# Performance work log

Hardware: AMD Instinct MI355X
Metric: run time of the kernel (lower is better)

## Reference

```python
import jax, jax.numpy as jnp
import numpy as np

B, NR, NP, E, F, EIN, H, OUT = 2, 16384, 65536, 262144, 128, 4, 16, 4
EPS = 1e-6

def _mlp(x, W1, b1, W2, b2):
    return jax.nn.swish(x @ W1 + b1) @ W2 + b2

def _cond_norm(x, tau, C1, c1, C2, c2):
    # conditioned LayerNorm: scale/shift computed from tau by a shallow MLP
    h = jax.nn.swish(tau @ C1 + c1)               # [B, H]
    scale, shift = jnp.split(h @ C2 + c2, 2, -1)  # [B, F] each
    mu = jnp.mean(x, -1, keepdims=True)
    var = jnp.var(x, -1, keepdims=True)
    xn = (x - mu) * jax.lax.rsqrt(var + EPS)
    return xn * (1.0 + scale[:, None, :]) + shift[:, None, :]

def _segment_mean(feat, recv, num_segments):
    seg = lambda f, r: jax.ops.segment_sum(f, r, num_segments=num_segments)
    s = jax.vmap(seg)(feat, recv)
    cnt = jax.vmap(seg)(jnp.ones(recv.shape, feat.dtype), recv)
    return s / jnp.maximum(cnt, 1.0)[..., None]

def setup_inputs():
    key = jax.random.key(0)
    ks = iter(jax.random.split(key, 48))
    dense = lambda i, o: jax.random.normal(next(ks), (i, o), jnp.float32) / np.sqrt(i)
    inp = {}
    inp['rnode_features'] = jax.random.normal(next(ks), (B, NR, F), jnp.float32)
    inp['pnode_features'] = jax.random.normal(next(ks), (B, NP, F), jnp.float32)
    inp['edge_features'] = jax.random.normal(next(ks), (B, E, EIN), jnp.float32)
    inp['tau'] = jax.random.uniform(next(ks), (B, 1), jnp.float32)
    # edge embedding MLP + cond norm
    inp['We1'], inp['We2'] = dense(EIN, F), dense(F, F)
    inp['be1'], inp['be2'] = jnp.zeros((F,)), jnp.zeros((F,))
    inp['Ce1'], inp['Ce2'] = dense(1, H), dense(H, 2 * F)
    inp['ce1'], inp['ce2'] = jnp.zeros((H,)), jnp.zeros((2 * F,))
    # edge update MLP + cond norm
    inp['Wu1'], inp['Wu2'] = dense(3 * F, F), dense(F, F)
    inp['bu1'], inp['bu2'] = jnp.zeros((F,)), jnp.zeros((F,))
    inp['Cu1'], inp['Cu2'] = dense(1, H), dense(H, 2 * F)
    inp['cu1'], inp['cu2'] = jnp.zeros((H,)), jnp.zeros((2 * F,))
    # pnode update MLP + cond norm
    inp['Wp1'], inp['Wp2'] = dense(2 * F, F), dense(F, F)
    inp['bp1'], inp['bp2'] = jnp.zeros((F,)), jnp.zeros((F,))
    inp['Cp1'], inp['Cp2'] = dense(1, H), dense(H, 2 * F)
    inp['cp1'], inp['cp2'] = jnp.zeros((H,)), jnp.zeros((2 * F,))
    # rnode update MLP + cond norm
    inp['Wr1'], inp['Wr2'] = dense(F, F), dense(F, F)
    inp['br1'], inp['br2'] = jnp.zeros((F,)), jnp.zeros((F,))
    inp['Cr1'], inp['Cr2'] = dense(1, H), dense(H, 2 * F)
    inp['cr1'], inp['cr2'] = jnp.zeros((H,)), jnp.zeros((2 * F,))
    # pnode output MLP (no norm)
    inp['Wo1'], inp['Wo2'] = dense(F, F), dense(F, OUT)
    inp['bo1'], inp['bo2'] = jnp.zeros((F,)), jnp.zeros((OUT,))
    inp['senders'] = jax.random.randint(next(ks), (B, E), 0, NR, jnp.int32)
    inp['receivers'] = jax.random.randint(next(ks), (B, E), 0, NP, jnp.int32)
    return inp

def reference(rnode_features, pnode_features, edge_features, tau,
              We1, be1, We2, be2, Ce1, ce1, Ce2, ce2,
              Wu1, bu1, Wu2, bu2, Cu1, cu1, Cu2, cu2,
              Wp1, bp1, Wp2, bp2, Cp1, cp1, Cp2, cp2,
              Wr1, br1, Wr2, br2, Cr1, cr1, Cr2, cr2,
              Wo1, bo1, Wo2, bo2, senders, receivers):
    # 1) embed raw r2p edge features to latent size (embed_edges=True)
    e = _cond_norm(_mlp(edge_features, We1, be1, We2, be2), tau, Ce1, ce1, Ce2, ce2)
    # 2) one message-passing step: edge update from gathered sender/receiver feats
    sf = jnp.take_along_axis(rnode_features, senders[..., None], axis=1)    # [B,E,F]
    rf = jnp.take_along_axis(pnode_features, receivers[..., None], axis=1)  # [B,E,F]
    e = e + _cond_norm(_mlp(jnp.concatenate([e, sf, rf], -1), Wu1, bu1, Wu2, bu2),
                       tau, Cu1, cu1, Cu2, cu2)
    # 3) pnode update with segment_mean aggregation, residual
    agg = _segment_mean(e, receivers, NP)                                   # [B,NP,F]
    p = pnode_features + _cond_norm(
        _mlp(jnp.concatenate([pnode_features, agg], -1), Wp1, bp1, Wp2, bp2),
        tau, Cp1, cp1, Cp2, cp2)
    # 4) rnode update (no incoming edges; structurally present but unused by output)
    r = rnode_features + _cond_norm(_mlp(rnode_features, Wr1, br1, Wr2, br2),
                                    tau, Cr1, cr1, Cr2, cr2)
    del r
    # 5) output MLP on pnodes (node_output_size=dict(pnodes=num_outputs))
    return _mlp(p, Wo1, bo1, Wo2, bo2)
```

## Files before the change

kernel.cpp:

```cpp
#include <hip/hip_runtime.h>

constexpr int cB  = 2;
constexpr int cNR = 16384;
constexpr int cNP = 65536;
constexpr int cE  = 262144;
constexpr int cF  = 128;
constexpr int cEB = cE / 64;
constexpr int SP  = 136;
constexpr int EFP = 40;

typedef unsigned short u16;
using f32x4 = __attribute__((ext_vector_type(4))) float;
using s8v   = __attribute__((ext_vector_type(8))) short;

constexpr int G8_We2 = 0, G8_Wu1 = 16, G8_Wu2 = 64, G8_Wp1 = 80, G8_Wp2 = 112, G8_Wo1 = 128;
constexpr int G8_TOT = 144;
constexpr int SWZ_N = G8_TOT * 128 + 256 + 512;
constexpr int WB_WE1 = (G8_TOT * 128 + 256) * 8;

constexpr size_t WS_CNT  = 0;
constexpr size_t WS_POS  = WS_CNT + (size_t)cB * cNP;
constexpr size_t WS_BSUM = WS_POS + (size_t)cB * cNP;
constexpr size_t WS_SS   = WS_BSUM + 512;
constexpr size_t WS_WB   = WS_SS + 3 * cB * 256;
constexpr size_t WS_RB   = WS_WB + (size_t)SWZ_N * 4;
constexpr size_t WS_PB   = WS_RB + (size_t)cB * cNR * cF / 2;
constexpr size_t WS_EL   = WS_PB + (size_t)cB * cNP * cF / 2;
constexpr size_t WS_EB   = WS_EL + (size_t)cB * cE;

__device__ __forceinline__ float bf2f(u16 u) {
  union { unsigned int i; float f; } v; v.i = ((unsigned int)u) << 16; return v.f;
}
__device__ __forceinline__ u16 f2bf(float f) {
  union { float f; unsigned int i; } v; v.f = f;
  unsigned int x = v.i;
  return (u16)((x + 0x7fffu + ((x >> 16) & 1u)) >> 16);
}
__device__ __forceinline__ u16 f2bf_fast(float f) {
  return (u16)((__float_as_uint(f) + 0x8000u) >> 16);
}
__device__ __forceinline__ unsigned pack2(float a, float b) {
  return __builtin_amdgcn_perm(__float_as_uint(b) + 0x8000u,
                               __float_as_uint(a) + 0x8000u, 0x07060302u);
}
__device__ __forceinline__ float swishf(float x) {
  return x * __builtin_amdgcn_rcpf(1.0f + __expf(-x));
}

template <int CTRL>
__device__ __forceinline__ float dpp_add(float x) {
  int xi = __float_as_int(x);
  int r = __builtin_amdgcn_update_dpp(xi, xi, CTRL, 0xf, 0xf, false);
  return x + __int_as_float(r);
}

__device__ __forceinline__ void gload4_lds(const u16* gsrc, u16* lds) {
  __builtin_amdgcn_global_load_lds(
      (const __attribute__((address_space(1))) void*)gsrc,
      (__attribute__((address_space(3))) void*)lds, 4, 0, 0);
}

__device__ __forceinline__ void kloop128s(const u16* act, const u16* __restrict__ wbg,
                                          f32x4 (&acc)[4][2], int cw, int l16, int quad) {
  s8v bf[4][2];
#pragma unroll
  for (int k0 = 0; k0 < 4; ++k0)
#pragma unroll
    for (int ci = 0; ci < 2; ++ci)
      bf[k0][ci] = *(const s8v*)(wbg + ((size_t)(k0 * 4 + quad) * 128 + cw + ci * 16 + l16) * 8);
#pragma unroll
  for (int k0 = 0; k0 < 4; ++k0) {
    s8v af[4];
#pragma unroll
    for (int ri = 0; ri < 4; ++ri)
      af[ri] = *(const s8v*)(act + (ri * 16 + l16) * SP + k0 * 32 + quad * 8);
#pragma unroll
    for (int ri = 0; ri < 4; ++ri)
#pragma unroll
      for (int ci = 0; ci < 2; ++ci)
        acc[ri][ci] = __builtin_amdgcn_mfma_f32_16x16x32_bf16(af[ri], bf[k0][ci], acc[ri][ci], 0, 0, 0);
  }
}

__device__ __forceinline__ void init_acc_s(f32x4 (&acc)[4][2], const float* __restrict__ bias,
                                           int cw, int l16) {
#pragma unroll
  for (int ci = 0; ci < 2; ++ci) {
    float bv = bias[cw + ci * 16 + l16];
#pragma unroll
    for (int ri = 0; ri < 4; ++ri) acc[ri][ci] = (f32x4){bv, bv, bv, bv};
  }
}

__device__ __forceinline__ void cond_norm_s(f32x4 (&acc)[4][2], float* red, float* musig,
                                            const float* __restrict__ ssp,
                                            int cw, int l16, int quad, int wv, int t) {
  __syncthreads();
#pragma unroll
  for (int ri = 0; ri < 4; ++ri)
#pragma unroll
    for (int reg = 0; reg < 4; ++reg) {
      float v0 = acc[ri][0][reg], v1 = acc[ri][1][reg];
      float s = v0 + v1;
      float q = v0 * v0 + v1 * v1;
      s = dpp_add<0x128>(s); q = dpp_add<0x128>(q);
      s = dpp_add<0x124>(s); q = dpp_add<0x124>(q);
      s = dpp_add<0x122>(s); q = dpp_add<0x122>(q);
      s = dpp_add<0x121>(s); q = dpp_add<0x121>(q);
      if (l16 == 0) {
        int row = ri * 16 + quad * 4 + reg;
        red[row * 8 + wv * 2]     = s;
        red[row * 8 + wv * 2 + 1] = q;
      }
    }
  __syncthreads();
  if (t < 64) {
    float sum = red[t * 8 + 0] + red[t * 8 + 2] + red[t * 8 + 4] + red[t * 8 + 6];
    float sq  = red[t * 8 + 1] + red[t * 8 + 3] + red[t * 8 + 5] + red[t * 8 + 7];
    float mu  = sum * (1.0f / 128.0f);
    float var = fmaxf(sq * (1.0f / 128.0f) - mu * mu, 0.0f);
    musig[t * 2]     = mu;
    musig[t * 2 + 1] = __builtin_amdgcn_rsqf(var + 1e-6f);
  }
  __syncthreads();
  float scl[2], shf[2];
#pragma unroll
  for (int ci = 0; ci < 2; ++ci) {
    int col = cw + ci * 16 + l16;
    scl[ci] = 1.0f + ssp[col];
    shf[ci] = ssp[128 + col];
  }
#pragma unroll
  for (int ri = 0; ri < 4; ++ri)
#pragma unroll
    for (int reg = 0; reg < 4; ++reg) {
      int row = ri * 16 + quad * 4 + reg;
      float mu = musig[row * 2], is = musig[row * 2 + 1];
#pragma unroll
      for (int ci = 0; ci < 2; ++ci)
        acc[ri][ci][reg] = (acc[ri][ci][reg] - mu) * is * scl[ci] + shf[ci];
    }
}

template <bool DOSWISH>
__device__ __forceinline__ void store_s(u16* buf, const f32x4 (&acc)[4][2],
                                        int cw, int l16, int quad) {
#pragma unroll
  for (int ri = 0; ri < 4; ++ri)
#pragma unroll
    for (int reg = 0; reg < 4; ++reg) {
      int row = ri * 16 + quad * 4 + reg;
#pragma unroll
      for (int ci = 0; ci < 2; ++ci) {
        float v = acc[ri][ci][reg];
        if (DOSWISH) v = swishf(v);
        buf[row * SP + cw + ci * 16 + l16] = f2bf_fast(v);
      }
    }
}

__global__ void zero_kernel(float4* __restrict__ p, int n4) {
  int i = blockIdx.x * 256 + threadIdx.x;
  if (i < n4) p[i] = make_float4(0.f, 0.f, 0.f, 0.f);
}

__global__ void cvtn2_kernel(const float* __restrict__ sa, u16* __restrict__ da, int n2a,
                             const float* __restrict__ sb, u16* __restrict__ db, int n2b) {
  int i = blockIdx.x * 256 + threadIdx.x;
  if (i < n2a) {
    float2 v = ((const float2*)sa)[i];
    ((unsigned*)da)[i] = pack2(v.x, v.y);
  } else if (i < n2a + n2b) {
    int k = i - n2a;
    float2 v = ((const float2*)sb)[k];
    ((unsigned*)db)[k] = pack2(v.x, v.y);
  }
}

__global__ void hist_kernel(const int* __restrict__ receivers, int* __restrict__ cntI) {
  int i = blockIdx.x * 256 + threadIdx.x;
  if (i >= cB * cE) return;
  int b = i / cE;
  int r = min(max(receivers[i], 0), cNP - 1);
  atomicAdd(&cntI[(size_t)b * cNP + r], 1);
}

__global__ void scanA_kernel(const int* __restrict__ cntI, int* __restrict__ bsum) {
  __shared__ int red[256];
  int g = blockIdx.x, t = threadIdx.x;
  red[t] = cntI[g * 256 + t];
  __syncthreads();
  for (int s = 128; s > 0; s >>= 1) {
    if (t < s) red[t] += red[t + s];
    __syncthreads();
  }
  if (t == 0) bsum[g] = red[0];
}

__global__ void scanB_kernel(int* __restrict__ bsum) {
  __shared__ int s0[512], s1[512];
  int t = threadIdx.x;
  int v0 = bsum[t];
  s0[t] = v0;
  __syncthreads();
  int* src = s0; int* dst = s1;
  for (int s = 1; s < 512; s <<= 1) {
    dst[t] = src[t] + ((t >= s) ? src[t - s] : 0);
    __syncthreads();
    int* tmp = src; src = dst; dst = tmp;
  }
  bsum[t] = src[t] - v0;
}

__global__ void scanC_kernel(const int* __restrict__ cntI, const int* __restrict__ bsum,
                             int* __restrict__ pos) {
  __shared__ int s0[256], s1[256];
  int g = blockIdx.x, t = threadIdx.x;
  int v0 = cntI[g * 256 + t];
  s0[t] = v0;
  __syncthreads();
  int* src = s0; int* dst = s1;
  for (int s = 1; s < 256; s <<= 1) {
    dst[t] = src[t] + ((t >= s) ? src[t - s] : 0);
    __syncthreads();
    int* tmp = src; src = dst; dst = tmp;
  }
  pos[g * 256 + t] = src[t] - v0 + bsum[g];
}

__global__ void fill_kernel(const int* __restrict__ receivers, int* __restrict__ pos,
                            int* __restrict__ elist) {
  int i = blockIdx.x * 256 + threadIdx.x;
  if (i >= cB * cE) return;
  int b = i / cE, e = i - b * cE;
  int r = min(max(receivers[i], 0), cNP - 1);
  int idx = atomicAdd(&pos[(size_t)b * cNP + r], 1);
  elist[idx] = e;
}

struct SwzSrc { const float* p[7]; };

__global__ void swz_kernel(SwzSrc s, const float* __restrict__ Wo2, u16* __restrict__ wb) {
  int t = blockIdx.x * 256 + threadIdx.x;
  if (t >= SWZ_N) return;
  if (t >= G8_TOT * 128 + 256) {
    int idx3 = t - (G8_TOT * 128 + 256);
    int k8 = idx3 >> 7, n = idx3 & 127;
    const float* We1 = s.p[6];
    u16 v[8];
#pragma unroll
    for (int j = 0; j < 8; ++j) {
      int k = k8 * 8 + j;
      v[j] = (k < 4) ? f2bf(We1[(size_t)k * 128 + n]) : (u16)0;
    }
    ((uint4*)wb)[t] = *(uint4*)v;
    return;
  }
  if (t >= G8_TOT * 128) {
    int idx2 = t - G8_TOT * 128;
    int k8 = idx2 >> 4, n = idx2 & 15;
    u16 v[8];
#pragma unroll
    for (int j = 0; j < 8; ++j)
      v[j] = (n < 4) ? f2bf(Wo2[(size_t)(k8 * 8 + j) * 4 + n]) : (u16)0;
    ((uint4*)wb)[G8_TOT * 128 + k8 * 16 + n] = *(uint4*)v;
    return;
  }
  int n = t & 127, g8 = t >> 7;
  int seg, base;
  if (g8 < G8_Wu1)      { seg = 0; base = G8_We2; }
  else if (g8 < G8_Wu2) { seg = 1; base = G8_Wu1; }
  else if (g8 < G8_Wp1) { seg = 2; base = G8_Wu2; }
  else if (g8 < G8_Wp2) { seg = 3; base = G8_Wp1; }
  else if (g8 < G8_Wo1) { seg = 4; base = G8_Wp2; }
  else                  { seg = 5; base = G8_Wo1; }
  const float* W = s.p[seg];
  int k8l = g8 - base;
  u16 v[8];
#pragma unroll
  for (int j = 0; j < 8; ++j) {
    int kd = k8l * 8 + j;
    int ks = kd;
    if (seg == 3 && kd >= 128) {
      int p = kd - 128;
      ks = 128 + ((p >> 5) << 5) + ((p & 1) << 4) + ((p & 31) >> 1);
    }
    v[j] = f2bf(W[(size_t)ks * 128 + n]);
  }
  ((uint4*)wb)[g8 * 128 + n] = *(uint4*)v;
}

__global__ void cond_kernel(const float* __restrict__ tau,
                            const float* __restrict__ Ce1, const float* __restrict__ ce1,
                            const float* __restrict__ Ce2, const float* __restrict__ ce2,
                            const float* __restrict__ Cu1, const float* __restrict__ cu1,
                            const float* __restrict__ Cu2, const float* __restrict__ cu2,
                            const float* __restrict__ Cp1, const float* __restrict__ cp1,
                            const float* __restrict__ Cp2, const float* __restrict__ cp2,
                            float* __restrict__ ss) {
  int set = blockIdx.x, b = blockIdx.y, j = threadIdx.x;
  const float *C1, *c1, *C2, *c2;
  if (set == 0)      { C1 = Ce1; c1 = ce1; C2 = Ce2; c2 = ce2; }
  else if (set == 1) { C1 = Cu1; c1 = cu1; C2 = Cu2; c2 = cu2; }
  else               { C1 = Cp1; c1 = cp1; C2 = Cp2; c2 = cp2; }
  float tf = tau[b];
  float a = c2[j];
  for (int k = 0; k < 16; ++k) {
    float h = swishf(tf * C1[k] + c1[k]);
    a = fmaf(h, C2[k * 256 + j], a);
  }
  ss[(size_t)set * cB * 256 + (size_t)b * 256 + j] = a;
}

struct EWb { const float *be1, *be2, *bu1, *bu2; };

struct __align__(16) EdgeSmem {
  u16 bufE[64 * SP];
  u16 bufX[64 * SP];
  union {
    u16 ef[64 * EFP];
    struct { float red[512]; float musig[128]; } r;
  } u;
  int sidx[64], ridx[64];
};

__global__ __launch_bounds__(256, 4) void edge_mfma(
    const u16* __restrict__ rnb, const u16* __restrict__ pnb,
    const float* __restrict__ efeat, const int* __restrict__ senders,
    const int* __restrict__ receivers, const int* __restrict__ elist,
    EWb w, const u16* __restrict__ wb,
    const float* __restrict__ ss, u16* __restrict__ ebuf) {
  __shared__ EdgeSmem sm;
  const int t = threadIdx.x, wv = t >> 6, lane = t & 63, l16 = lane & 15, quad = lane >> 4;
  const int cw = wv * 32;
  const int raw = blockIdx.x;
  const int swz = (raw & 7) * (cB * cEB / 8) + (raw >> 3);
  const int b   = swz / cEB;

  if (t < 64) {
    int eid = elist[(size_t)swz * 64 + t];
    size_t ge = (size_t)b * cE + eid;
    sm.sidx[t] = min(max(senders[ge], 0), cNR - 1);
    sm.ridx[t] = min(max(receivers[ge], 0), cNP - 1);
    float4 ef = *(const float4*)(efeat + ge * 4);
    uint4 w0 = { pack2(ef.x, ef.y), pack2(ef.z, ef.w), 0u, 0u };
    uint4 zz = { 0u, 0u, 0u, 0u };
    uint4* rowp = (uint4*)(sm.u.ef + (size_t)t * EFP);
    rowp[0] = w0; rowp[1] = zz; rowp[2] = zz; rowp[3] = zz; rowp[4] = zz;
  }
  __syncthreads();

  f32x4 acc[4][2];

  init_acc_s(acc, w.be1, cw, l16);
  {
    const u16* wbe1 = wb + WB_WE1;
    s8v bf0 = *(const s8v*)(wbe1 + ((size_t)quad * 128 + cw + l16) * 8);
    s8v bf1 = *(const s8v*)(wbe1 + ((size_t)quad * 128 + cw + 16 + l16) * 8);
#pragma unroll
    for (int ri = 0; ri < 4; ++ri) {
      s8v af = *(const s8v*)(sm.u.ef + (ri * 16 + l16) * EFP + quad * 8);
      acc[ri][0] = __builtin_amdgcn_mfma_f32_16x16x32_bf16(af, bf0, acc[ri][0], 0, 0, 0);
      acc[ri][1] = __builtin_amdgcn_mfma_f32_16x16x32_bf16(af, bf1, acc[ri][1], 0, 0, 0);
    }
  }
  store_s<true>(sm.bufX, acc, cw, l16, quad);
  __syncthreads();

  init_acc_s(acc, w.be2, cw, l16);
  kloop128s(sm.bufX, wb + (size_t)G8_We2 * 1024, acc, cw, l16, quad);
  cond_norm_s(acc, sm.u.r.red, sm.u.r.musig, ss + (size_t)b * 256, cw, l16, quad, wv, t);
  store_s<false>(sm.bufE, acc, cw, l16, quad);

#pragma unroll
  for (int rr = 0; rr < 16; ++rr) {
    int row = wv * 16 + rr;
    int si = __builtin_amdgcn_readfirstlane(sm.sidx[row]);
    gload4_lds(rnb + ((size_t)b * cNR + si) * cF + lane * 2,
               sm.bufX + row * SP);
  }
  f32x4 accU[4][2];
  init_acc_s(accU, w.bu1, cw, l16);
  __syncthreads();
  kloop128s(sm.bufX, wb + (size_t)(G8_Wu1 + 16) * 1024, accU, cw, l16, quad);
  __syncthreads();
#pragma unroll
  for (int rr = 0; rr < 16; ++rr) {
    int row = wv * 16 + rr;
    int ri_ = __builtin_amdgcn_readfirstlane(sm.ridx[row]);
    gload4_lds(pnb + ((size_t)b * cNP + ri_) * cF + lane * 2,
               sm.bufX + row * SP);
  }
  kloop128s(sm.bufE, wb + (size_t)G8_Wu1 * 1024, accU, cw, l16, quad);
  __syncthreads();
  kloop128s(sm.bufX, wb + (size_t)(G8_Wu1 + 32) * 1024, accU, cw, l16, quad);
  __syncthreads();
  store_s<true>(sm.bufX, accU, cw, l16, quad);
  __syncthreads();

  init_acc_s(acc, w.bu2, cw, l16);
  kloop128s(sm.bufX, wb + (size_t)G8_Wu2 * 1024, acc, cw, l16, quad);
  cond_norm_s(acc, sm.u.r.red, sm.u.r.musig, ss + (size_t)(cB + b) * 256, cw, l16, quad, wv, t);

  {
    unsigned* eb32o = (unsigned*)ebuf + (size_t)(swz * 64) * 64;
#pragma unroll
    for (int ri = 0; ri < 4; ++ri)
#pragma unroll
      for (int reg = 0; reg < 4; ++reg) {
        int row = ri * 16 + quad * 4 + reg;
        float v0 = acc[ri][0][reg] + bf2f(sm.bufE[row * SP + cw + l16]);
        float v1 = acc[ri][1][reg] + bf2f(sm.bufE[row * SP + cw + 16 + l16]);
        eb32o[(size_t)row * 64 + wv * 16 + l16] = pack2(v0, v1);
      }
  }
}

struct PWb { const float *bp1, *bp2, *bo1, *bo2; };

struct __align__(16) PnodeSmem {
  u16 bufP[64 * SP];
  u16 bufX[64 * SP];
  float red[512];
  float musig[128];
  float cinv[64];
  int startA[64];
  int endA[72];
};

__global__ __launch_bounds__(256, 4) void pnode_mfma(
    const u16* __restrict__ pnb, PWb w, const u16* __restrict__ wb,
    const float* __restrict__ ss, const unsigned* __restrict__ eb32,
    const int* __restrict__ cntI, const int* __restrict__ pos,
    float* __restrict__ out) {
  __shared__ PnodeSmem sm;
  const int t = threadIdx.x, wv = t >> 6, lane = t & 63, l16 = lane & 15, quad = lane >> 4;
  const int cw = wv * 32;
  const int b  = blockIdx.y;
  const int n0 = blockIdx.x * 64;

  if (t < 64) {
    size_t g = (size_t)b * cNP + n0 + t;
    int c  = cntI[g];
    int e_ = pos[g];
    sm.startA[t] = e_ - c;
    sm.endA[t]   = e_;
    sm.cinv[t]   = __builtin_amdgcn_rcpf(fmaxf((float)c, 1.0f));
  } else if (t < 72) {
    sm.endA[t] = 0x7fffffff;
  }
  __syncthreads();

#pragma unroll
  for (int rr = 0; rr < 16; ++rr) {
    int row = wv * 16 + rr;
    unsigned pvu = *(const unsigned*)(pnb + (((size_t)b * cNP + n0 + row) * cF + lane * 2));
    *(unsigned*)(sm.bufP + row * SP + lane * 2) = pvu;
  }

  {
    const int nodeLo = wv * 16;
    int cur  = nodeLo;
    int bnd  = __builtin_amdgcn_readfirstlane(sm.endA[cur]);
    int s    = __builtin_amdgcn_readfirstlane(sm.startA[nodeLo]);
    const int sEnd = __builtin_amdgcn_readfirstlane(sm.endA[nodeLo + 15]);
    float a0 = 0.f, a1 = 0.f;
    for (; s < sEnd; s += 8) {
      unsigned v[8];
      int m = sEnd - s;
#pragma unroll
      for (int j = 0; j < 8; ++j)
        if (j < m) v[j] = eb32[(size_t)(s + j) * 64 + lane];
#pragma unroll
      for (int j = 0; j < 8; ++j) {
        if (j < m) {
          while (s + j == bnd) {
            float ci = sm.cinv[cur];
            *(unsigned*)(sm.bufX + cur * SP + lane * 2) = pack2(a0 * ci, a1 * ci);
            a0 = a1 = 0.f; ++cur;
            bnd = __builtin_amdgcn_readfirstlane(sm.endA[cur]);
          }
          a0 += bf2f((u16)(v[j] & 0xffffu));
          a1 += bf2f((u16)(v[j] >> 16));
        }
      }
    }
    while (cur < nodeLo + 16) {
      float ci = sm.cinv[cur];
      *(unsigned*)(sm.bufX + cur * SP + lane * 2) = pack2(a0 * ci, a1 * ci);
      a0 = a1 = 0.f; ++cur;
    }
  }
  __syncthreads();

  f32x4 acc[4][2];

  init_acc_s(acc, w.bp1, cw, l16);
  kloop128s(sm.bufP, wb + (size_t)G8_Wp1 * 1024, acc, cw, l16, quad);
  kloop128s(sm.bufX, wb + (size_t)(G8_Wp1 + 16) * 1024, acc, cw, l16, quad);
  __syncthreads();
  store_s<true>(sm.bufX, acc, cw, l16, quad);
  __syncthreads();

  init_acc_s(acc, w.bp2, cw, l16);
  kloop128s(sm.bufX, wb + (size_t)G8_Wp2 * 1024, acc, cw, l16, quad);
  cond_norm_s(acc, sm.red, sm.musig, ss + (size_t)(2 * cB + b) * 256, cw, l16, quad, wv, t);
#pragma unroll
  for (int ri = 0; ri < 4; ++ri)
#pragma unroll
    for (int reg = 0; reg < 4; ++reg) {
      int row = ri * 16 + quad * 4 + reg;
#pragma unroll
      for (int ci = 0; ci < 2; ++ci)
        acc[ri][ci][reg] += bf2f(sm.bufP[row * SP + cw + ci * 16 + l16]);
    }
  __syncthreads();
  store_s<false>(sm.bufP, acc, cw, l16, quad);
  __syncthreads();

  init_acc_s(acc, w.bo1, cw, l16);
  kloop128s(sm.bufP, wb + (size_t)G8_Wo1 * 1024, acc, cw, l16, quad);
  store_s<true>(sm.bufX, acc, cw, l16, quad);
  __syncthreads();

  {
    const u16* wo2 = wb + (size_t)G8_TOT * 1024;
    float bv = (l16 < 4) ? w.bo2[l16] : 0.0f;
    f32x4 a1 = {bv, bv, bv, bv};
#pragma unroll
    for (int k0 = 0; k0 < 4; ++k0) {
      s8v af = *(const s8v*)(sm.bufX + (wv * 16 + l16) * SP + k0 * 32 + quad * 8);
      s8v bf = *(const s8v*)(wo2 + ((size_t)(k0 * 4 + quad) * 16 + l16) * 8);
      a1 = __builtin_amdgcn_mfma_f32_16x16x32_bf16(af, bf, a1, 0, 0, 0);
    }
    if (l16 < 4) {
      size_t obase = (size_t)b * cNP + n0 + wv * 16 + quad * 4;
#pragma unroll
      for (int reg = 0; reg < 4; ++reg)
        out[(obase + reg) * 4 + l16] = a1[reg];
    }
  }
}

extern "C" void kernel_launch(void* const* d_in, const int* in_sizes, int n_in,
                              void* d_out, int out_size, void* d_ws, size_t ws_size,
                              hipStream_t stream) {
  const float* rnode = (const float*)d_in[0];
  const float* pnode = (const float*)d_in[1];
  const float* efeat = (const float*)d_in[2];
  const float* tau   = (const float*)d_in[3];
  const int* senders   = (const int*)d_in[40];
  const int* receivers = (const int*)d_in[41];
  float* ws = (float*)d_ws;
  int* cntI  = (int*)(ws + WS_CNT);
  int* pos   = (int*)(ws + WS_POS);
  int* bsum  = (int*)(ws + WS_BSUM);
  u16* wb    = (u16*)(ws + WS_WB);
  u16* rnb   = (u16*)(ws + WS_RB);
  u16* pnb   = (u16*)(ws + WS_PB);
  int* elist = (int*)(ws + WS_EL);
  u16* ebuf  = (u16*)(ws + WS_EB);

  SwzSrc sw;
  sw.p[0] = (const float*)d_in[5];
  sw.p[1] = (const float*)d_in[12];
  sw.p[2] = (const float*)d_in[13];
  sw.p[3] = (const float*)d_in[20];
  sw.p[4] = (const float*)d_in[21];
  sw.p[5] = (const float*)d_in[36];
  sw.p[6] = (const float*)d_in[4];
  swz_kernel<<<(SWZ_N + 255) / 256, 256, 0, stream>>>(sw, (const float*)d_in[37], wb);

  const int nrn2 = (int)((size_t)cB * cNR * cF / 2);
  const int npn2 = (int)((size_t)cB * cNP * cF / 2);
  cvtn2_kernel<<<(nrn2 + npn2 + 255) / 256, 256, 0, stream>>>(
      rnode, rnb, nrn2, pnode, pnb, npn2);

  cond_kernel<<<dim3(3, cB), 256, 0, stream>>>(
      tau,
      (const float*)d_in[8],  (const float*)d_in[10],
      (const float*)d_in[9],  (const float*)d_in[11],
      (const float*)d_in[16], (const float*)d_in[18],
      (const float*)d_in[17], (const float*)d_in[19],
      (const float*)d_in[24], (const float*)d_in[26],
      (const float*)d_in[25], (const float*)d_in[27],
      ws + WS_SS);

  const int n4 = (int)((size_t)cB * cNP * 4 / 16);
  zero_kernel<<<(n4 + 255) / 256, 256, 0, stream>>>((float4*)cntI, n4);
  const int nBE = cB * cE;
  hist_kernel<<<(nBE + 255) / 256, 256, 0, stream>>>(receivers, cntI);
  scanA_kernel<<<512, 256, 0, stream>>>(cntI, bsum);
  scanB_kernel<<<1, 512, 0, stream>>>(bsum);
  scanC_kernel<<<512, 256, 0, stream>>>(cntI, bsum, pos);
  fill_kernel<<<(nBE + 255) / 256, 256, 0, stream>>>(receivers, pos, elist);

  EWb ew = { (const float*)d_in[6], (const float*)d_in[7],
             (const float*)d_in[14], (const float*)d_in[15] };
  PWb pw = { (const float*)d_in[22], (const float*)d_in[23], (const float*)d_in[38],
             (const float*)d_in[39] };

  edge_mfma<<<dim3(cB * cEB), 256, 0, stream>>>(
      rnb, pnb, efeat, senders, receivers, elist, ew, wb,
      ws + WS_SS, ebuf);

  pnode_mfma<<<dim3(cNP / 64, cB), 256, 0, stream>>>(
      pnb, pw, wb, ws + WS_SS, (const unsigned*)ebuf, cntI, pos,
      (float*)d_out);
}
```

Baseline: 456.4 us.

## Split edge and pnode MFMA work across eight waves with sixteen columns each

The edge and pnode kernels go from 4 waves of 256 threads, each owning 32 output columns, to 8 waves of 512 threads, each owning 16 columns. The reduction buffer grows to hold 8 partial sums, and gathers and segment sums are split over 8 rows per wave. The edge kernel now stages its residual output through LDS and writes rows with coalesced stores instead of scattered packed stores. The Wp1 row permutation is dropped from weight packing, which only stays consistent if that permutation matched the old 2-column interleaved store. The aim is more waves to hide latency, at the cost of more barriers and duplicated activation-fragment loads per MFMA.

```diff
diff --git a/kernel.cpp b/kernel.cpp
--- a/kernel.cpp
+++ b/kernel.cpp
@@ -60,39 +60,30 @@
       (__attribute__((address_space(3))) void*)lds, 4, 0, 0);
 }
 
-__device__ __forceinline__ void kloop128s(const u16* act, const u16* __restrict__ wbg,
-                                          f32x4 (&acc)[4][2], int cw, int l16, int quad) {
-  s8v bf[4][2];
+__device__ __forceinline__ void kloop16(const u16* act, const u16* __restrict__ wbg,
+                                        f32x4 (&acc)[4], int cw, int l16, int quad) {
+  s8v bf[4];
 #pragma unroll
   for (int k0 = 0; k0 < 4; ++k0)
-#pragma unroll
-    for (int ci = 0; ci < 2; ++ci)
-      bf[k0][ci] = *(const s8v*)(wbg + ((size_t)(k0 * 4 + quad) * 128 + cw + ci * 16 + l16) * 8);
+    bf[k0] = *(const s8v*)(wbg + ((size_t)(k0 * 4 + quad) * 128 + cw + l16) * 8);
 #pragma unroll
   for (int k0 = 0; k0 < 4; ++k0) {
-    s8v af[4];
-#pragma unroll
-    for (int ri = 0; ri < 4; ++ri)
-      af[ri] = *(const s8v*)(act + (ri * 16 + l16) * SP + k0 * 32 + quad * 8);
-#pragma unroll
-    for (int ri = 0; ri < 4; ++ri)
-#pragma unroll
-      for (int ci = 0; ci < 2; ++ci)
-        acc[ri][ci] = __builtin_amdgcn_mfma_f32_16x16x32_bf16(af[ri], bf[k0][ci], acc[ri][ci], 0, 0, 0);
-  }
-}
-
-__device__ __forceinline__ void init_acc_s(f32x4 (&acc)[4][2], const float* __restrict__ bias,
+#pragma unroll
+    for (int ri = 0; ri < 4; ++ri) {
+      s8v af = *(const s8v*)(act + (ri * 16 + l16) * SP + k0 * 32 + quad * 8);
+      acc[ri] = __builtin_amdgcn_mfma_f32_16x16x32_bf16(af, bf[k0], acc[ri], 0, 0, 0);
+    }
+  }
+}
+
+__device__ __forceinline__ void init_acc16(f32x4 (&acc)[4], const float* __restrict__ bias,
                                            int cw, int l16) {
-#pragma unroll
-  for (int ci = 0; ci < 2; ++ci) {
-    float bv = bias[cw + ci * 16 + l16];
-#pragma unroll
-    for (int ri = 0; ri < 4; ++ri) acc[ri][ci] = (f32x4){bv, bv, bv, bv};
-  }
-}
-
-__device__ __forceinline__ void cond_norm_s(f32x4 (&acc)[4][2], float* red, float* musig,
+  float bv = bias[cw + l16];
+#pragma unroll
+  for (int ri = 0; ri < 4; ++ri) acc[ri] = (f32x4){bv, bv, bv, bv};
+}
+
+__device__ __forceinline__ void cond_norm16(f32x4 (&acc)[4], float* red, float* musig,
                                             const float* __restrict__ ssp,
                                             int cw, int l16, int quad, int wv, int t) {
   __syncthreads();
@@ -100,62 +91,56 @@
   for (int ri = 0; ri < 4; ++ri)
 #pragma unroll
     for (int reg = 0; reg < 4; ++reg) {
-      float v0 = acc[ri][0][reg], v1 = acc[ri][1][reg];
-      float s = v0 + v1;
-      float q = v0 * v0 + v1 * v1;
+      float v = acc[ri][reg];
+      float s = v;
+      float q = v * v;
       s = dpp_add<0x128>(s); q = dpp_add<0x128>(q);
       s = dpp_add<0x124>(s); q = dpp_add<0x124>(q);
       s = dpp_add<0x122>(s); q = dpp_add<0x122>(q);
       s = dpp_add<0x121>(s); q = dpp_add<0x121>(q);
       if (l16 == 0) {
         int row = ri * 16 + quad * 4 + reg;
-        red[row * 8 + wv * 2]     = s;
-        red[row * 8 + wv * 2 + 1] = q;
+        red[row * 16 + wv * 2]     = s;
+        red[row * 16 + wv * 2 + 1] = q;
       }
     }
   __syncthreads();
   if (t < 64) {
-    float sum = red[t * 8 + 0] + red[t * 8 + 2] + red[t * 8 + 4] + red[t * 8 + 6];
-    float sq  = red[t * 8 + 1] + red[t * 8 + 3] + red[t * 8 + 5] + red[t * 8 + 7];
+    float sum = 0.f, sq = 0.f;
+#pragma unroll
+    for (int w8 = 0; w8 < 8; ++w8) {
+      sum += red[t * 16 + w8 * 2];
+      sq  += red[t * 16 + w8 * 2 + 1];
+    }
     float mu  = sum * (1.0f / 128.0f);
     float var = fmaxf(sq * (1.0f / 128.0f) - mu * mu, 0.0f);
     musig[t * 2]     = mu;
     musig[t * 2 + 1] = __builtin_amdgcn_rsqf(var + 1e-6f);
   }
   __syncthreads();
-  float scl[2], shf[2];
-#pragma unroll
-  for (int ci = 0; ci < 2; ++ci) {
-    int col = cw + ci * 16 + l16;
-    scl[ci] = 1.0f + ssp[col];
-    shf[ci] = ssp[128 + col];
-  }
+  float scl = 1.0f + ssp[cw + l16];
+  float shf = ssp[128 + cw + l16];
 #pragma unroll
   for (int ri = 0; ri < 4; ++ri)
 #pragma unroll
     for (int reg = 0; reg < 4; ++reg) {
       int row = ri * 16 + quad * 4 + reg;
       float mu = musig[row * 2], is = musig[row * 2 + 1];
-#pragma unroll
-      for (int ci = 0; ci < 2; ++ci)
-        acc[ri][ci][reg] = (acc[ri][ci][reg] - mu) * is * scl[ci] + shf[ci];
+      acc[ri][reg] = (acc[ri][reg] - mu) * is * scl + shf;
     }
 }
 
 template <bool DOSWISH>
-__device__ __forceinline__ void store_s(u16* buf, const f32x4 (&acc)[4][2],
+__device__ __forceinline__ void store16(u16* buf, const f32x4 (&acc)[4],
                                         int cw, int l16, int quad) {
 #pragma unroll
   for (int ri = 0; ri < 4; ++ri)
 #pragma unroll
     for (int reg = 0; reg < 4; ++reg) {
       int row = ri * 16 + quad * 4 + reg;
-#pragma unroll
-      for (int ci = 0; ci < 2; ++ci) {
-        float v = acc[ri][ci][reg];
-        if (DOSWISH) v = swishf(v);
-        buf[row * SP + cw + ci * 16 + l16] = f2bf_fast(v);
-      }
+      float v = acc[ri][reg];
+      if (DOSWISH) v = swishf(v);
+      buf[row * SP + cw + l16] = f2bf_fast(v);
     }
 }
 
@@ -278,15 +263,7 @@
   int k8l = g8 - base;
   u16 v[8];
 #pragma unroll
-  for (int j = 0; j < 8; ++j) {
-    int kd = k8l * 8 + j;
-    int ks = kd;
-    if (seg == 3 && kd >= 128) {
-      int p = kd - 128;
-      ks = 128 + ((p >> 5) << 5) + ((p & 1) << 4) + ((p & 31) >> 1);
-    }
-    v[j] = f2bf(W[(size_t)ks * 128 + n]);
-  }
+  for (int j = 0; j < 8; ++j) v[j] = f2bf(W[(size_t)(k8l * 8 + j) * 128 + n]);
   ((uint4*)wb)[g8 * 128 + n] = *(uint4*)v;
 }
 
@@ -319,12 +296,12 @@
   u16 bufX[64 * SP];
   union {
     u16 ef[64 * EFP];
-    struct { float red[512]; float musig[128]; } r;
+    struct { float red[1024]; float musig[128]; } r;
   } u;
   int sidx[64], ridx[64];
 };
 
-__global__ __launch_bounds__(256, 4) void edge_mfma(
+__global__ __launch_bounds__(512, 8) void edge_mfma(
     const u16* __restrict__ rnb, const u16* __restrict__ pnb,
     const float* __restrict__ efeat, const int* __restrict__ senders,
     const int* __restrict__ receivers, const int* __restrict__ elist,
@@ -332,7 +309,7 @@
     const float* __restrict__ ss, u16* __restrict__ ebuf) {
   __shared__ EdgeSmem sm;
   const int t = threadIdx.x, wv = t >> 6, lane = t & 63, l16 = lane & 15, quad = lane >> 4;
-  const int cw = wv * 32;
+  const int cw = wv * 16;
   const int raw = blockIdx.x;
   const int swz = (raw & 7) * (cB * cEB / 8) + (raw >> 3);
   const int b   = swz / cEB;
@@ -350,69 +327,73 @@
   }
   __syncthreads();
 
-  f32x4 acc[4][2];
-
-  init_acc_s(acc, w.be1, cw, l16);
+  f32x4 acc[4];
+
+  init_acc16(acc, w.be1, cw, l16);
   {
     const u16* wbe1 = wb + WB_WE1;
     s8v bf0 = *(const s8v*)(wbe1 + ((size_t)quad * 128 + cw + l16) * 8);
-    s8v bf1 = *(const s8v*)(wbe1 + ((size_t)quad * 128 + cw + 16 + l16) * 8);
 #pragma unroll
     for (int ri = 0; ri < 4; ++ri) {
       s8v af = *(const s8v*)(sm.u.ef + (ri * 16 + l16) * EFP + quad * 8);
-      acc[ri][0] = __builtin_amdgcn_mfma_f32_16x16x32_bf16(af, bf0, acc[ri][0], 0, 0, 0);
-      acc[ri][1] = __builtin_amdgcn_mfma_f32_16x16x32_bf16(af, bf1, acc[ri][1], 0, 0, 0);
-    }
-  }
-  store_s<true>(sm.bufX, acc, cw, l16, quad);
-  __syncthreads();
-
-  init_acc_s(acc, w.be2, cw, l16);
-  kloop128s(sm.bufX, wb + (size_t)G8_We2 * 1024, acc, cw, l16, quad);
-  cond_norm_s(acc, sm.u.r.red, sm.u.r.musig, ss + (size_t)b * 256, cw, l16, quad, wv, t);
-  store_s<false>(sm.bufE, acc, cw, l16, quad);
-
-#pragma unroll
-  for (int rr = 0; rr < 16; ++rr) {
-    int row = wv * 16 + rr;
+      acc[ri] = __builtin_amdgcn_mfma_f32_16x16x32_bf16(af, bf0, acc[ri], 0, 0, 0);
+    }
+  }
+  store16<true>(sm.bufX, acc, cw, l16, quad);
+  __syncthreads();
+
+  init_acc16(acc, w.be2, cw, l16);
+  kloop16(sm.bufX, wb + (size_t)G8_We2 * 1024, acc, cw, l16, quad);
+  cond_norm16(acc, sm.u.r.red, sm.u.r.musig, ss + (size_t)b * 256, cw, l16, quad, wv, t);
+  store16<false>(sm.bufE, acc, cw, l16, quad);
+
+#pragma unroll
+  for (int rr = 0; rr < 8; ++rr) {
+    int row = wv * 8 + rr;
     int si = __builtin_amdgcn_readfirstlane(sm.sidx[row]);
     gload4_lds(rnb + ((size_t)b * cNR + si) * cF + lane * 2,
                sm.bufX + row * SP);
   }
-  f32x4 accU[4][2];
-  init_acc_s(accU, w.bu1, cw, l16);
-  __syncthreads();
-  kloop128s(sm.bufX, wb + (size_t)(G8_Wu1 + 16) * 1024, accU, cw, l16, quad);
-  __syncthreads();
-#pragma unroll
-  for (int rr = 0; rr < 16; ++rr) {
-    int row = wv * 16 + rr;
+  f32x4 accU[4];
+  init_acc16(accU, w.bu1, cw, l16);
+  __syncthreads();
+  kloop16(sm.bufX, wb + (size_t)(G8_Wu1 + 16) * 1024, accU, cw, l16, quad);
+  __syncthreads();
+#pragma unroll
+  for (int rr = 0; rr < 8; ++rr) {
+    int row = wv * 8 + rr;
     int ri_ = __builtin_amdgcn_readfirstlane(sm.ridx[row]);
     gload4_lds(pnb + ((size_t)b * cNP + ri_) * cF + lane * 2,
                sm.bufX + row * SP);
   }
-  kloop128s(sm.bufE, wb + (size_t)G8_Wu1 * 1024, accU, cw, l16, quad);
-  __syncthreads();
-  kloop128s(sm.bufX, wb + (size_t)(G8_Wu1 + 32) * 1024, accU, cw, l16, quad);
-  __syncthreads();
-  store_s<true>(sm.bufX, accU, cw, l16, quad);
-  __syncthreads();
-
-  init_acc_s(acc, w.bu2, cw, l16);
-  kloop128s(sm.bufX, wb + (size_t)G8_Wu2 * 1024, acc, cw, l16, quad);
-  cond_norm_s(acc, sm.u.r.red, sm.u.r.musig, ss + (size_t)(cB + b) * 256, cw, l16, quad, wv, t);
-
+  kloop16(sm.bufE, wb + (size_t)G8_Wu1 * 1024, accU, cw, l16, quad);
+  __syncthreads();
+  kloop16(sm.bufX, wb + (size_t)(G8_Wu1 + 32) * 1024, accU, cw, l16, quad);
+  __syncthreads();
+  store16<true>(sm.bufX, accU, cw, l16, quad);
+  __syncthreads();
+
+  init_acc16(acc, w.bu2, cw, l16);
+  kloop16(sm.bufX, wb + (size_t)G8_Wu2 * 1024, acc, cw, l16, quad);
+  cond_norm16(acc, sm.u.r.red, sm.u.r.musig, ss + (size_t)(cB + b) * 256, cw, l16, quad, wv, t);
+
+#pragma unroll
+  for (int ri = 0; ri < 4; ++ri)
+#pragma unroll
+    for (int reg = 0; reg < 4; ++reg) {
+      int row = ri * 16 + quad * 4 + reg;
+      acc[ri][reg] += bf2f(sm.bufE[row * SP + cw + l16]);
+    }
+  store16<false>(sm.bufX, acc, cw, l16, quad);
+  __syncthreads();
   {
     unsigned* eb32o = (unsigned*)ebuf + (size_t)(swz * 64) * 64;
 #pragma unroll
-    for (int ri = 0; ri < 4; ++ri)
-#pragma unroll
-      for (int reg = 0; reg < 4; ++reg) {
-        int row = ri * 16 + quad * 4 + reg;
-        float v0 = acc[ri][0][reg] + bf2f(sm.bufE[row * SP + cw + l16]);
-        float v1 = acc[ri][1][reg] + bf2f(sm.bufE[row * SP + cw + 16 + l16]);
-        eb32o[(size_t)row * 64 + wv * 16 + l16] = pack2(v0, v1);
-      }
+    for (int rr = 0; rr < 8; ++rr) {
+      int row = wv * 8 + rr;
+      unsigned v = *(const unsigned*)(sm.bufX + row * SP + lane * 2);
+      eb32o[(size_t)row * 64 + lane] = v;
+    }
   }
 }
 
@@ -421,21 +402,21 @@
 struct __align__(16) PnodeSmem {
   u16 bufP[64 * SP];
   u16 bufX[64 * SP];
-  float red[512];
+  float red[1024];
   float musig[128];
   float cinv[64];
   int startA[64];
   int endA[72];
 };
 
-__global__ __launch_bounds__(256, 4) void pnode_mfma(
+__global__ __launch_bounds__(512, 8) void pnode_mfma(
     const u16* __restrict__ pnb, PWb w, const u16* __restrict__ wb,
     const float* __restrict__ ss, const unsigned* __restrict__ eb32,
     const int* __restrict__ cntI, const int* __restrict__ pos,
     float* __restrict__ out) {
   __shared__ PnodeSmem sm;
   const int t = threadIdx.x, wv = t >> 6, lane = t & 63, l16 = lane & 15, quad = lane >> 4;
-  const int cw = wv * 32;
+  const int cw = wv * 16;
   const int b  = blockIdx.y;
   const int n0 = blockIdx.x * 64;
 
@@ -452,18 +433,18 @@
   __syncthreads();
 
 #pragma unroll
-  for (int rr = 0; rr < 16; ++rr) {
-    int row = wv * 16 + rr;
+  for (int rr = 0; rr < 8; ++rr) {
+    int row = wv * 8 + rr;
     unsigned pvu = *(const unsigned*)(pnb + (((size_t)b * cNP + n0 + row) * cF + lane * 2));
     *(unsigned*)(sm.bufP + row * SP + lane * 2) = pvu;
   }
 
   {
-    const int nodeLo = wv * 16;
+    const int nodeLo = wv * 8;
     int cur  = nodeLo;
     int bnd  = __builtin_amdgcn_readfirstlane(sm.endA[cur]);
     int s    = __builtin_amdgcn_readfirstlane(sm.startA[nodeLo]);
-    const int sEnd = __builtin_amdgcn_readfirstlane(sm.endA[nodeLo + 15]);
+    const int sEnd = __builtin_amdgcn_readfirstlane(sm.endA[nodeLo + 7]);
     float a0 = 0.f, a1 = 0.f;
     for (; s < sEnd; s += 8) {
       unsigned v[8];
@@ -485,7 +466,7 @@
         }
       }
     }
-    while (cur < nodeLo + 16) {
+    while (cur < nodeLo + 8) {
       float ci = sm.cinv[cur];
       *(unsigned*)(sm.bufX + cur * SP + lane * 2) = pack2(a0 * ci, a1 * ci);
       a0 = a1 = 0.f; ++cur;
@@ -493,37 +474,35 @@
   }
   __syncthreads();
 
-  f32x4 acc[4][2];
-
-  init_acc_s(acc, w.bp1, cw, l16);
-  kloop128s(sm.bufP, wb + (size_t)G8_Wp1 * 1024, acc, cw, l16, quad);
-  kloop128s(sm.bufX, wb + (size_t)(G8_Wp1 + 16) * 1024, acc, cw, l16, quad);
-  __syncthreads();
-  store_s<true>(sm.bufX, acc, cw, l16, quad);
-  __syncthreads();
-
-  init_acc_s(acc, w.bp2, cw, l16);
-  kloop128s(sm.bufX, wb + (size_t)G8_Wp2 * 1024, acc, cw, l16, quad);
-  cond_norm_s(acc, sm.red, sm.musig, ss + (size_t)(2 * cB + b) * 256, cw, l16, quad, wv, t);
+  f32x4 acc[4];
+
+  init_acc16(acc, w.bp1, cw, l16);
+  kloop16(sm.bufP, wb + (size_t)G8_Wp1 * 1024, acc, cw, l16, quad);
+  kloop16(sm.bufX, wb + (size_t)(G8_Wp1 + 16) * 1024, acc, cw, l16, quad);
+  __syncthreads();
+  store16<true>(sm.bufX, acc, cw, l16, quad);
+  __syncthreads();
+
+  init_acc16(acc, w.bp2, cw, l16);
+  kloop16(sm.bufX, wb + (size_t)G8_Wp2 * 1024, acc, cw, l16, quad);
+  cond_norm16(acc, sm.red, sm.musig, ss + (size_t)(2 * cB + b) * 256, cw, l16, quad, wv, t);
 #pragma unroll
   for (int ri = 0; ri < 4; ++ri)
 #pragma unroll
     for (int reg = 0; reg < 4; ++reg) {
       int row = ri * 16 + quad * 4 + reg;
-#pragma unroll
-      for (int ci = 0; ci < 2; ++ci)
-        acc[ri][ci][reg] += bf2f(sm.bufP[row * SP + cw + ci * 16 + l16]);
-    }
-  __syncthreads();
-  store_s<false>(sm.bufP, acc, cw, l16, quad);
-  __syncthreads();
-
-  init_acc_s(acc, w.bo1, cw, l16);
-  kloop128s(sm.bufP, wb + (size_t)G8_Wo1 * 1024, acc, cw, l16, quad);
-  store_s<true>(sm.bufX, acc, cw, l16, quad);
-  __syncthreads();
-
-  {
+      acc[ri][reg] += bf2f(sm.bufP[row * SP + cw + l16]);
+    }
+  __syncthreads();
+  store16<false>(sm.bufP, acc, cw, l16, quad);
+  __syncthreads();
+
+  init_acc16(acc, w.bo1, cw, l16);
+  kloop16(sm.bufP, wb + (size_t)G8_Wo1 * 1024, acc, cw, l16, quad);
+  store16<true>(sm.bufX, acc, cw, l16, quad);
+  __syncthreads();
+
+  if (wv < 4) {
     const u16* wo2 = wb + (size_t)G8_TOT * 1024;
     float bv = (l16 < 4) ? w.bo2[l16] : 0.0f;
     f32x4 a1 = {bv, bv, bv, bv};
@@ -600,11 +579,11 @@
   PWb pw = { (const float*)d_in[22], (const float*)d_in[23], (const float*)d_in[38],
              (const float*)d_in[39] };
 
-  edge_mfma<<<dim3(cB * cEB), 256, 0, stream>>>(
+  edge_mfma<<<dim3(cB * cEB), 512, 0, stream>>>(
       rnb, pnb, efeat, senders, receivers, elist, ew, wb,
       ws + WS_SS, ebuf);
 
-  pnode_mfma<<<dim3(cNP / 64, cB), 256, 0, stream>>>(
+  pnode_mfma<<<dim3(cNP / 64, cB), 512, 0, stream>>>(
       pnb, pw, wb, ws + WS_SS, (const unsigned*)ebuf, cntI, pos,
       (float*)d_out);
 }
```

After: 488.5 us. 1.07x slower.
